# Kernel optimization log

Hardware: AMD Instinct MI355X
Metric: run time of the kernel (lower is better)

The kernel has to match this reference:

```python
import jax, jax.numpy as jnp
import numpy as np

B, T, D = 8, 1024, 768
N_HEAD = 12
HEAD_DIM = D // N_HEAD


def setup_inputs() -> dict:
    key = jax.random.key(0)
    k1, k2, k3, k4, k5 = jax.random.split(key, 5)
    x = jax.random.normal(k1, (B, T, D), dtype=jnp.float32)
    # c_attn: Linear(D, 3D); c_proj: Linear(D, D). Stored as (in, out) for x @ W.
    s_attn = 1.0 / np.sqrt(D)
    W_attn = jax.random.uniform(k2, (D, 3 * D), dtype=jnp.float32, minval=-s_attn, maxval=s_attn)
    b_attn = jax.random.uniform(k3, (3 * D,), dtype=jnp.float32, minval=-s_attn, maxval=s_attn)
    W_proj = jax.random.uniform(k4, (D, D), dtype=jnp.float32, minval=-s_attn, maxval=s_attn)
    b_proj = jax.random.uniform(k5, (D,), dtype=jnp.float32, minval=-s_attn, maxval=s_attn)
    return {"x": x, "W_attn": W_attn, "b_attn": b_attn, "W_proj": W_proj, "b_proj": b_proj}


def reference(x, W_attn, b_attn, W_proj, b_proj):
    Bs, Ts, Ds = x.shape
    qkv = x @ W_attn + b_attn  # [B, T, 3D]
    Q, K, V = jnp.split(qkv, 3, axis=2)
    # [B, H, T, hd]
    Q = Q.reshape(Bs, Ts, N_HEAD, HEAD_DIM).transpose(0, 2, 1, 3)
    K = K.reshape(Bs, Ts, N_HEAD, HEAD_DIM).transpose(0, 2, 1, 3)
    V = V.reshape(Bs, Ts, N_HEAD, HEAD_DIM).transpose(0, 2, 1, 3)
    scale = HEAD_DIM ** (-0.5)
    scores = jnp.einsum('bhqd,bhkd->bhqk', Q, K) * scale  # [B, H, T, T]
    causal = jnp.tril(jnp.ones((Ts, Ts), dtype=bool))
    scores = jnp.where(causal[None, None, :, :], scores, -jnp.inf)
    probs = jax.nn.softmax(scores, axis=-1)
    attn = jnp.einsum('bhqk,bhkd->bhqd', probs, V)  # [B, H, T, hd]
    attn = attn.transpose(0, 2, 1, 3).reshape(Bs, Ts, Ds)
    return attn @ W_proj + b_proj
```

## Files before the change

kernel.cpp:

```cpp
#include <hip/hip_runtime.h>
#include <hip/hip_bf16.h>

#define B_ 8
#define T_ 1024
#define D_ 768
#define NH 12
#define HD 64

typedef __bf16 bf16x8 __attribute__((ext_vector_type(8)));
typedef __bf16 bf16x4 __attribute__((ext_vector_type(4)));
typedef float f32x4 __attribute__((ext_vector_type(4)));
typedef short s16x4 __attribute__((ext_vector_type(4)));

__device__ __forceinline__ float fast_exp2(float x) {
  return __builtin_amdgcn_exp2f(x);
}

__device__ __forceinline__ f32x4 mfma32(bf16x8 a, bf16x8 b, f32x4 c) {
  return __builtin_amdgcn_mfma_f32_16x16x32_bf16(a, b, c, 0, 0, 0);
}

__device__ __forceinline__ f32x4 mfma16(bf16x4 a, bf16x4 b, f32x4 c) {
  union U { bf16x4 h; s16x4 s; };
  U ua; ua.h = a;
  U ub; ub.h = b;
  return __builtin_amdgcn_mfma_f32_16x16x16bf16_1k(ua.s, ub.s, c, 0, 0, 0);
}

__device__ __forceinline__ void gload_lds16(const void* g, void* l) {
  __builtin_amdgcn_global_load_lds((const __attribute__((address_space(1))) unsigned int*)g,
                                   (__attribute__((address_space(3))) unsigned int*)l, 16, 0, 0);
}

__global__ void xconv_kernel(const float* __restrict__ x, __bf16* __restrict__ xb, int n8) {
  int i = blockIdx.x * 256 + threadIdx.x;
  if (i >= n8) return;
  const float4* xf = (const float4*)x;
  float4 a = xf[i * 2], b = xf[i * 2 + 1];
  bf16x8 v;
  v[0] = (__bf16)a.x; v[1] = (__bf16)a.y; v[2] = (__bf16)a.z; v[3] = (__bf16)a.w;
  v[4] = (__bf16)b.x; v[5] = (__bf16)b.y; v[6] = (__bf16)b.z; v[7] = (__bf16)b.w;
  *(bf16x8*)&xb[(size_t)i * 8] = v;
}

__global__ void wtrans_kernel(const float* __restrict__ W, __bf16* __restrict__ WT, int K, int N) {
  __shared__ float tile[32][33];
  int t = threadIdx.x, col = t & 31, r0 = t >> 5;
  int n0 = blockIdx.x * 32, k0 = blockIdx.y * 32;
#pragma unroll
  for (int p = 0; p < 4; p++) {
    int r = r0 + p * 8;
    tile[r][col] = W[(size_t)(k0 + r) * N + n0 + col];
  }
  __syncthreads();
#pragma unroll
  for (int p = 0; p < 4; p++) {
    int r = r0 + p * 8;
    WT[(size_t)(n0 + r) * K + k0 + col] = (__bf16)tile[col][r];
  }
}

template <int EPI>
__global__ __launch_bounds__(256) void gemm_kernel(const __bf16* __restrict__ A,
                                                   const __bf16* __restrict__ BT,
                                                   const float* __restrict__ bias,
                                                   void* __restrict__ Cout,
                                                   int M, int N, int K, int nbx) {
  __shared__ __align__(16) __bf16 Asm[2][128 * 64];
  __shared__ __align__(16) __bf16 Bsm[2][128 * 64];
  int tid = threadIdx.x;
  int wave = tid >> 6, lane = tid & 63, g = lane >> 4, l15 = lane & 15;
  int wr = wave >> 1, wc = wave & 1;

  int wg = blockIdx.x;
  int cpx = gridDim.x >> 3;
  int wg2 = (wg & 7) * cpx + (wg >> 3);
  int bx = wg2 % nbx, by = wg2 / nbx;
  int m0 = by * 128, n0 = bx * 128;

  int srow = tid >> 3;
  int cc = (tid & 7) ^ ((tid >> 3) & 7);
  const __bf16* Ag = A + (size_t)(m0 + srow) * K + cc * 8;
  const __bf16* Bg = BT + (size_t)(n0 + srow) * K + cc * 8;

  auto stage = [&](int kt, int bf) {
#pragma unroll
    for (int i = 0; i < 4; i++) {
      gload_lds16(Ag + (size_t)(i * 32) * K + kt * 64, &Asm[bf][wave * 512 + i * 2048]);
      gload_lds16(Bg + (size_t)(i * 32) * K + kt * 64, &Bsm[bf][wave * 512 + i * 2048]);
    }
  };

  f32x4 zz = {0.0f, 0.0f, 0.0f, 0.0f};
  f32x4 acc[4][4];
#pragma unroll
  for (int m = 0; m < 4; m++)
#pragma unroll
    for (int n = 0; n < 4; n++) acc[m][n] = zz;

  int nk = K >> 6;
  int swr = l15 & 7;

  stage(0, 0);
  __syncthreads();

  int cur = 0;
  for (int kt = 0; kt < nk; kt++) {
    if (kt + 1 < nk) stage(kt + 1, cur ^ 1);
#pragma unroll
    for (int ks = 0; ks < 2; ks++) {
      bf16x8 af[4], bfr[4];
#pragma unroll
      for (int m = 0; m < 4; m++) {
        int row = wr * 64 + m * 16 + l15;
        af[m] = *(const bf16x8*)&Asm[cur][row * 64 + ((ks * 4 + g) ^ swr) * 8];
      }
#pragma unroll
      for (int n = 0; n < 4; n++) {
        int row = wc * 64 + n * 16 + l15;
        bfr[n] = *(const bf16x8*)&Bsm[cur][row * 64 + ((ks * 4 + g) ^ swr) * 8];
      }
#pragma unroll
      for (int m = 0; m < 4; m++)
#pragma unroll
        for (int n = 0; n < 4; n++)
          acc[m][n] = __builtin_amdgcn_mfma_f32_16x16x32_bf16(af[m], bfr[n], acc[m][n], 0, 0, 0);
    }
    __syncthreads();
    cur ^= 1;
  }
#pragma unroll
  for (int n = 0; n < 4; n++) {
    int gcol = n0 + wc * 64 + n * 16 + l15;
    float bv = bias[gcol];
#pragma unroll
    for (int m = 0; m < 4; m++) {
      int grow0 = m0 + wr * 64 + m * 16 + g * 4;
#pragma unroll
      for (int r = 0; r < 4; r++) {
        float v = acc[m][n][r] + bv;
        if (EPI == 0)
          ((__bf16*)Cout)[(size_t)(grow0 + r) * N + gcol] = (__bf16)v;
        else
          ((float*)Cout)[(size_t)(grow0 + r) * N + gcol] = v;
      }
    }
  }
}

__global__ void vtrepack_kernel(const __bf16* __restrict__ qkv, __bf16* __restrict__ VT) {
  __shared__ __align__(16) __bf16 tl[64][72];
  int bh = blockIdx.y;
  int b = bh / NH, h = bh % NH;
  int t0 = blockIdx.x * 64;
  int tid = threadIdx.x;
  int tr = tid >> 3, d8 = tid & 7;
#pragma unroll
  for (int p = 0; p < 2; p++) {
    int trow = tr + p * 32;
    bf16x8 v = *(const bf16x8*)&qkv[(size_t)(b * T_ + t0 + trow) * (3 * D_) + 2 * D_ + h * HD + d8 * 8];
#pragma unroll
    for (int e = 0; e < 8; e++) tl[d8 * 8 + e][trow] = v[e];
  }
  __syncthreads();
  int t8 = tid & 7;
#pragma unroll
  for (int p = 0; p < 2; p++) {
    int d = (tid >> 3) + p * 32;
    *(bf16x8*)&VT[((size_t)bh * HD + d) * T_ + t0 + t8 * 8] = *(const bf16x8*)&tl[d][t8 * 8];
  }
}

#define SCL 0.1803368801111204f

__global__ __launch_bounds__(256, 4) void attn_kernel(const __bf16* __restrict__ qkv,
                                                      const __bf16* __restrict__ VT,
                                                      __bf16* __restrict__ attn_out) {
  __shared__ __align__(16) __bf16 sm[2][2][4096];
  int tid = threadIdx.x;
  int wave = tid >> 6, lane = tid & 63, g = lane >> 4, l15 = lane & 15;
  int bh = blockIdx.x;
  int b = bh / NH, h = bh % NH;
  int qb = 15 - blockIdx.y;
  int q0w = qb * 64 + wave * 16;
  int nkt = qb + 1;
  int s0 = (bh + qb) % nkt;

  int kr = tid >> 3, cc = (tid & 7) ^ ((tid >> 3) & 7);
  const __bf16* Kst = qkv + (size_t)(b * T_ + kr) * (3 * D_) + D_ + h * HD + cc * 8;
  const __bf16* Vst = VT + ((size_t)bh * HD + kr) * T_ + cc * 8;
  __bf16* ldsK0 = &sm[0][0][wave * 512];
  __bf16* ldsV0 = &sm[0][1][wave * 512];
  __bf16* ldsK1 = &sm[1][0][wave * 512];
  __bf16* ldsV1 = &sm[1][1][wave * 512];

  auto stage = [&](int t, int bf) {
    size_t ko = (size_t)(t * 64) * (3 * D_);
    int vo = t * 64;
    __bf16* lk = bf ? ldsK1 : ldsK0;
    __bf16* lv = bf ? ldsV1 : ldsV0;
    gload_lds16(Kst + ko, lk);
    gload_lds16(Kst + ko + (size_t)32 * (3 * D_), lk + 2048);
    gload_lds16(Vst + vo, lv);
    gload_lds16(Vst + vo + 32 * T_, lv + 2048);
  };

  const __bf16* Qp = qkv + (size_t)(b * T_ + q0w + l15) * (3 * D_) + h * HD;
  bf16x8 qlo = *(const bf16x8*)(Qp + g * 8);
  bf16x8 qhi = *(const bf16x8*)(Qp + 32 + g * 8);

  f32x4 zz = {0.0f, 0.0f, 0.0f, 0.0f};
  f32x4 o0 = zz, o1 = zz, o2 = zz, o3 = zz;
  float m = -1e30f, l = 0.0f;
  int sw = l15 & 7;
  int clo = (g ^ sw) * 8;
  int chi = ((4 + g) ^ sw) * 8;

  stage(s0, 0);
  __syncthreads();

  int cur = 0;
  for (int i = 0; i < nkt; i++) {
    int kt = s0 + i;
    if (kt >= nkt) kt -= nkt;
    if (i + 1 < nkt) stage(kt + 1 == nkt ? 0 : kt + 1, cur ^ 1);

    const __bf16* Kb = &sm[cur][0][0];
    f32x4 s[4];
#pragma unroll
    for (int kg = 0; kg < 4; kg++) {
      int rb = (kg * 16 + l15) * 64;
      bf16x8 kf = *(const bf16x8*)(Kb + rb + clo);
      bf16x8 kh = *(const bf16x8*)(Kb + rb + chi);
      s[kg] = mfma32(kf, qlo, zz);
      s[kg] = mfma32(kh, qhi, s[kg]);
    }

    float v[16];
#pragma unroll
    for (int kg = 0; kg < 4; kg++)
#pragma unroll
      for (int r = 0; r < 4; r++) v[kg * 4 + r] = s[kg][r] * SCL;
    if (kt == qb) {
      int thr = wave * 16 + l15;
#pragma unroll
      for (int kg = 0; kg < 4; kg++)
#pragma unroll
        for (int r = 0; r < 4; r++)
          if (kg * 16 + g * 4 + r > thr) v[kg * 4 + r] = -1e30f;
    }
    float m0a = fmaxf(fmaxf(v[0], v[1]), fmaxf(v[2], v[3]));
    float m1a = fmaxf(fmaxf(v[4], v[5]), fmaxf(v[6], v[7]));
    float m2a = fmaxf(fmaxf(v[8], v[9]), fmaxf(v[10], v[11]));
    float m3a = fmaxf(fmaxf(v[12], v[13]), fmaxf(v[14], v[15]));
    float mx = fmaxf(fmaxf(m0a, m1a), fmaxf(m2a, m3a));
    mx = fmaxf(mx, __shfl_xor(mx, 16));
    mx = fmaxf(mx, __shfl_xor(mx, 32));
    float mnew = fmaxf(m, mx);
    float corr = fast_exp2(m - mnew);
    float p[16], sum = 0.0f;
#pragma unroll
    for (int i2 = 0; i2 < 16; i2++) { p[i2] = fast_exp2(v[i2] - mnew); sum += p[i2]; }
    sum += __shfl_xor(sum, 16);
    sum += __shfl_xor(sum, 32);
    l = l * corr + sum;
    m = mnew;
    o0 *= corr; o1 *= corr; o2 *= corr; o3 *= corr;
    bf16x4 pk[4];
#pragma unroll
    for (int kg = 0; kg < 4; kg++) {
      pk[kg][0] = (__bf16)p[kg * 4 + 0];
      pk[kg][1] = (__bf16)p[kg * 4 + 1];
      pk[kg][2] = (__bf16)p[kg * 4 + 2];
      pk[kg][3] = (__bf16)p[kg * 4 + 3];
    }

    const __bf16* Vb = &sm[cur][1][0];
    int vhalf = (g & 1) * 4;
    int vc = g >> 1;
#pragma unroll
    for (int dq = 0; dq < 4; dq++) {
      int drow = (dq * 16 + l15) * 64;
#pragma unroll
      for (int ks = 0; ks < 4; ks++) {
        bf16x4 vf = *(const bf16x4*)(Vb + drow + ((ks * 2 + vc) ^ sw) * 8 + vhalf);
        f32x4* op = (dq == 0) ? &o0 : (dq == 1) ? &o1 : (dq == 2) ? &o2 : &o3;
        *op = mfma16(vf, pk[ks], *op);
      }
    }

    __syncthreads();
    cur ^= 1;
  }

  float invl = 1.0f / l;
  __bf16* outp = attn_out + (size_t)(b * T_ + q0w + l15) * D_ + h * HD + g * 4;
  bf16x4 t0 = {(__bf16)(o0[0] * invl), (__bf16)(o0[1] * invl), (__bf16)(o0[2] * invl), (__bf16)(o0[3] * invl)};
  bf16x4 t1 = {(__bf16)(o1[0] * invl), (__bf16)(o1[1] * invl), (__bf16)(o1[2] * invl), (__bf16)(o1[3] * invl)};
  bf16x4 t2 = {(__bf16)(o2[0] * invl), (__bf16)(o2[1] * invl), (__bf16)(o2[2] * invl), (__bf16)(o2[3] * invl)};
  bf16x4 t3 = {(__bf16)(o3[0] * invl), (__bf16)(o3[1] * invl), (__bf16)(o3[2] * invl), (__bf16)(o3[3] * invl)};
  *(bf16x4*)(outp) = t0;
  *(bf16x4*)(outp + 16) = t1;
  *(bf16x4*)(outp + 32) = t2;
  *(bf16x4*)(outp + 48) = t3;
}

extern "C" void kernel_launch(void* const* d_in, const int* in_sizes, int n_in,
                              void* d_out, int out_size, void* d_ws, size_t ws_size,
                              hipStream_t stream) {
  (void)in_sizes; (void)n_in; (void)out_size; (void)ws_size;
  const float* x = (const float*)d_in[0];
  const float* W_attn = (const float*)d_in[1];
  const float* b_attn = (const float*)d_in[2];
  const float* W_proj = (const float*)d_in[3];
  const float* b_proj = (const float*)d_in[4];

  char* ws = (char*)d_ws;
  __bf16* xb  = (__bf16*)(ws + 0);
  __bf16* WaT = (__bf16*)(ws + 12582912);
  __bf16* WpT = (__bf16*)(ws + 16121856);
  __bf16* qkv = (__bf16*)(ws + 17301504);
  __bf16* VTb = (__bf16*)(ws + 55050240);
  __bf16* att = (__bf16*)(ws + 67633152);

  xconv_kernel<<<dim3(3072), 256, 0, stream>>>(x, xb, 786432);
  wtrans_kernel<<<dim3(72, 24), 256, 0, stream>>>(W_attn, WaT, 768, 2304);
  wtrans_kernel<<<dim3(24, 24), 256, 0, stream>>>(W_proj, WpT, 768, 768);
  gemm_kernel<0><<<dim3(1152), 256, 0, stream>>>(xb, WaT, b_attn, qkv, 8192, 2304, 768, 18);
  vtrepack_kernel<<<dim3(16, 96), 256, 0, stream>>>(qkv, VTb);
  attn_kernel<<<dim3(96, 16), 256, 0, stream>>>(qkv, VTb, att);
  gemm_kernel<1><<<dim3(384), 256, 0, stream>>>(att, WpT, b_proj, d_out, 8192, 768, 768, 6);
}
```

Before: 121.2 us.

## Fuse V transpose into QKV GEMM epilogue, refine pipeline waits, lazy softmax rescale

Removes the separate V-transpose kernel by having the QKV GEMM epilogue write the V columns straight into the transposed VT layout. The GEMM main loop now uses explicit vmcnt waits and raw barriers so the next tile's loads can stay in flight. In attention, the online softmax only rescales the accumulators when the running max grows by more than a threshold, and the MFMA sections get raised wave priority. Risks are uncoalesced bf16x4 scattered stores for VT, possible overflow headroom issues from the lazy rescale, and fragile hand-placed waitcnt counts.

```diff
diff --git a/kernel.cpp b/kernel.cpp
--- a/kernel.cpp
+++ b/kernel.cpp
@@ -65,6 +65,7 @@
                                                    const __bf16* __restrict__ BT,
                                                    const float* __restrict__ bias,
                                                    void* __restrict__ Cout,
+                                                   __bf16* __restrict__ VT,
                                                    int M, int N, int K, int nbx) {
   __shared__ __align__(16) __bf16 Asm[2][128 * 64];
   __shared__ __align__(16) __bf16 Bsm[2][128 * 64];
@@ -102,11 +103,16 @@
   int swr = l15 & 7;
 
   stage(0, 0);
-  __syncthreads();
 
   int cur = 0;
   for (int kt = 0; kt < nk; kt++) {
-    if (kt + 1 < nk) stage(kt + 1, cur ^ 1);
+    if (kt + 1 < nk) {
+      stage(kt + 1, cur ^ 1);
+      asm volatile("s_waitcnt vmcnt(8)" ::: "memory");
+    } else {
+      asm volatile("s_waitcnt vmcnt(0)" ::: "memory");
+    }
+    __builtin_amdgcn_s_barrier();
 #pragma unroll
     for (int ks = 0; ks < 2; ks++) {
       bf16x8 af[4], bfr[4];
@@ -126,7 +132,8 @@
         for (int n = 0; n < 4; n++)
           acc[m][n] = __builtin_amdgcn_mfma_f32_16x16x32_bf16(af[m], bfr[n], acc[m][n], 0, 0, 0);
     }
-    __syncthreads();
+    asm volatile("" ::: "memory");
+    __builtin_amdgcn_s_barrier();
     cur ^= 1;
   }
 #pragma unroll
@@ -136,38 +143,27 @@
 #pragma unroll
     for (int m = 0; m < 4; m++) {
       int grow0 = m0 + wr * 64 + m * 16 + g * 4;
-#pragma unroll
-      for (int r = 0; r < 4; r++) {
-        float v = acc[m][n][r] + bv;
-        if (EPI == 0)
-          ((__bf16*)Cout)[(size_t)(grow0 + r) * N + gcol] = (__bf16)v;
-        else
-          ((float*)Cout)[(size_t)(grow0 + r) * N + gcol] = v;
+      float v0 = acc[m][n][0] + bv, v1 = acc[m][n][1] + bv;
+      float v2 = acc[m][n][2] + bv, v3 = acc[m][n][3] + bv;
+      if (EPI == 1) {
+        float* C = (float*)Cout;
+        C[(size_t)(grow0 + 0) * N + gcol] = v0;
+        C[(size_t)(grow0 + 1) * N + gcol] = v1;
+        C[(size_t)(grow0 + 2) * N + gcol] = v2;
+        C[(size_t)(grow0 + 3) * N + gcol] = v3;
+      } else if (gcol < 2 * D_) {
+        __bf16* C = (__bf16*)Cout;
+        C[(size_t)(grow0 + 0) * N + gcol] = (__bf16)v0;
+        C[(size_t)(grow0 + 1) * N + gcol] = (__bf16)v1;
+        C[(size_t)(grow0 + 2) * N + gcol] = (__bf16)v2;
+        C[(size_t)(grow0 + 3) * N + gcol] = (__bf16)v3;
+      } else {
+        int hh = (gcol - 2 * D_) >> 6, dd = (gcol - 2 * D_) & 63;
+        int bb = grow0 >> 10, tt = grow0 & 1023;
+        bf16x4 sv = {(__bf16)v0, (__bf16)v1, (__bf16)v2, (__bf16)v3};
+        *(bf16x4*)&VT[((size_t)(bb * NH + hh) * HD + dd) * T_ + tt] = sv;
       }
     }
-  }
-}
-
-__global__ void vtrepack_kernel(const __bf16* __restrict__ qkv, __bf16* __restrict__ VT) {
-  __shared__ __align__(16) __bf16 tl[64][72];
-  int bh = blockIdx.y;
-  int b = bh / NH, h = bh % NH;
-  int t0 = blockIdx.x * 64;
-  int tid = threadIdx.x;
-  int tr = tid >> 3, d8 = tid & 7;
-#pragma unroll
-  for (int p = 0; p < 2; p++) {
-    int trow = tr + p * 32;
-    bf16x8 v = *(const bf16x8*)&qkv[(size_t)(b * T_ + t0 + trow) * (3 * D_) + 2 * D_ + h * HD + d8 * 8];
-#pragma unroll
-    for (int e = 0; e < 8; e++) tl[d8 * 8 + e][trow] = v[e];
-  }
-  __syncthreads();
-  int t8 = tid & 7;
-#pragma unroll
-  for (int p = 0; p < 2; p++) {
-    int d = (tid >> 3) + p * 32;
-    *(bf16x8*)&VT[((size_t)bh * HD + d) * T_ + t0 + t8 * 8] = *(const bf16x8*)&tl[d][t8 * 8];
   }
 }
 
@@ -227,6 +223,7 @@
 
     const __bf16* Kb = &sm[cur][0][0];
     f32x4 s[4];
+    __builtin_amdgcn_s_setprio(1);
 #pragma unroll
     for (int kg = 0; kg < 4; kg++) {
       int rb = (kg * 16 + l15) * 64;
@@ -235,6 +232,7 @@
       s[kg] = mfma32(kf, qlo, zz);
       s[kg] = mfma32(kh, qhi, s[kg]);
     }
+    __builtin_amdgcn_s_setprio(0);
 
     float v[16];
 #pragma unroll
@@ -256,16 +254,19 @@
     float mx = fmaxf(fmaxf(m0a, m1a), fmaxf(m2a, m3a));
     mx = fmaxf(mx, __shfl_xor(mx, 16));
     mx = fmaxf(mx, __shfl_xor(mx, 32));
-    float mnew = fmaxf(m, mx);
-    float corr = fast_exp2(m - mnew);
+    if (!__all(mx <= m + 8.0f)) {
+      float mnew = fmaxf(m, mx);
+      float corr = fast_exp2(m - mnew);
+      o0 *= corr; o1 *= corr; o2 *= corr; o3 *= corr;
+      l *= corr;
+      m = mnew;
+    }
     float p[16], sum = 0.0f;
 #pragma unroll
-    for (int i2 = 0; i2 < 16; i2++) { p[i2] = fast_exp2(v[i2] - mnew); sum += p[i2]; }
+    for (int i2 = 0; i2 < 16; i2++) { p[i2] = fast_exp2(v[i2] - m); sum += p[i2]; }
     sum += __shfl_xor(sum, 16);
     sum += __shfl_xor(sum, 32);
-    l = l * corr + sum;
-    m = mnew;
-    o0 *= corr; o1 *= corr; o2 *= corr; o3 *= corr;
+    l += sum;
     bf16x4 pk[4];
 #pragma unroll
     for (int kg = 0; kg < 4; kg++) {
@@ -278,6 +279,7 @@
     const __bf16* Vb = &sm[cur][1][0];
     int vhalf = (g & 1) * 4;
     int vc = g >> 1;
+    __builtin_amdgcn_s_setprio(1);
 #pragma unroll
     for (int dq = 0; dq < 4; dq++) {
       int drow = (dq * 16 + l15) * 64;
@@ -288,6 +290,7 @@
         *op = mfma16(vf, pk[ks], *op);
       }
     }
+    __builtin_amdgcn_s_setprio(0);
 
     __syncthreads();
     cur ^= 1;
@@ -326,8 +329,7 @@
   xconv_kernel<<<dim3(3072), 256, 0, stream>>>(x, xb, 786432);
   wtrans_kernel<<<dim3(72, 24), 256, 0, stream>>>(W_attn, WaT, 768, 2304);
   wtrans_kernel<<<dim3(24, 24), 256, 0, stream>>>(W_proj, WpT, 768, 768);
-  gemm_kernel<0><<<dim3(1152), 256, 0, stream>>>(xb, WaT, b_attn, qkv, 8192, 2304, 768, 18);
-  vtrepack_kernel<<<dim3(16, 96), 256, 0, stream>>>(qkv, VTb);
+  gemm_kernel<0><<<dim3(1152), 256, 0, stream>>>(xb, WaT, b_attn, qkv, VTb, 8192, 2304, 768, 18);
   attn_kernel<<<dim3(96, 16), 256, 0, stream>>>(qkv, VTb, att);
-  gemm_kernel<1><<<dim3(384), 256, 0, stream>>>(att, WpT, b_proj, d_out, 8192, 768, 768, 6);
-}
+  gemm_kernel<1><<<dim3(384), 256, 0, stream>>>(att, WpT, b_proj, d_out, nullptr, 8192, 768, 768, 6);
+}
```

Result: faster. 114.8 us (-5.3%).
